# Kernel optimization log

Measured on AMD Instinct MI355X. Metric: run time of the kernel, lower is better.

## Reference

```python
import jax, jax.numpy as jnp
import numpy as np

HIDDEN = 2048
NUM_HEADS = 16
HEAD_DIM = HIDDEN // NUM_HEADS
SCALE = 1.0 / np.sqrt(HEAD_DIM).astype(np.float32)
BATCH, SEQ = 2, 2048


def setup_inputs() -> dict:
    key = jax.random.key(0)
    ks = jax.random.split(key, 9)
    std = 0.02
    inp = {
        'hidden_states': jax.random.normal(ks[0], (BATCH, SEQ, HIDDEN), jnp.float32),
        'attention_mask': jnp.zeros((BATCH, 1, 1, SEQ), jnp.float32),
        'Wq': jax.random.normal(ks[1], (HIDDEN, HIDDEN), jnp.float32) * std,
        'bq': jnp.zeros((HIDDEN,), jnp.float32),
        'Wk': jax.random.normal(ks[2], (HIDDEN, HIDDEN), jnp.float32) * std,
        'bk': jnp.zeros((HIDDEN,), jnp.float32),
        'Wv': jax.random.normal(ks[3], (HIDDEN, HIDDEN), jnp.float32) * std,
        'bv': jnp.zeros((HIDDEN,), jnp.float32),
        'Wo': jax.random.normal(ks[4], (HIDDEN, HIDDEN), jnp.float32) * std,
        'bo': jnp.zeros((HIDDEN,), jnp.float32),
    }
    return inp


def _split_heads(x):
    b, s, _ = x.shape
    return x.reshape(b, s, NUM_HEADS, HEAD_DIM).transpose(0, 2, 1, 3)  # [b,h,s,d]


def reference(hidden_states, attention_mask, Wq, bq, Wk, bk, Wv, bv, Wo, bo):
    # Linear layers (torch convention: y = x @ W.T + b)
    q = _split_heads(hidden_states @ Wq.T + bq)
    k = _split_heads(hidden_states @ Wk.T + bk)
    v = _split_heads(hidden_states @ Wv.T + bv)
    scores = jnp.einsum('bhqd,bhkd->bhqk', q, k) * SCALE
    scores = scores + attention_mask
    weights = jax.nn.softmax(scores, axis=-1)  # dropout is identity in eval
    ctx = jnp.einsum('bhqk,bhkd->bhqd', weights, v)
    b, h, s, d = ctx.shape
    ctx = ctx.transpose(0, 2, 1, 3).reshape(b, s, HIDDEN)
    return ctx @ Wo.T + bo
```

## Files before the change

kernel.cpp:

```cpp
#include <hip/hip_runtime.h>
#include <math.h>

typedef __bf16 bf16_t;
typedef bf16_t bf16x8 __attribute__((ext_vector_type(8)));
typedef float f32x4 __attribute__((ext_vector_type(4)));

#define HIDDEN 2048
#define SEQ 2048
#define BATCH 2
#define NHEADS 16
#define HDIM 128
#define MTOT (BATCH*SEQ)
#define SCALE 0.088388347648318447f

typedef __attribute__((address_space(1))) const void gvoid_t;
typedef __attribute__((address_space(3))) void svoid_t;
__device__ __forceinline__ void async_copy16(const bf16_t* g, bf16_t* l) {
  __builtin_amdgcn_global_load_lds((gvoid_t*)g, (svoid_t*)l, 16, 0, 0);
}

__global__ void cvt_f32_bf16(const float* __restrict__ in, bf16_t* __restrict__ out, int n4) {
  int i = blockIdx.x * 256 + threadIdx.x;
  if (i >= n4) return;
  float4 v = reinterpret_cast<const float4*>(in)[i];
  union { bf16_t h[4]; uint2 u; } t;
  t.h[0] = (bf16_t)v.x; t.h[1] = (bf16_t)v.y; t.h[2] = (bf16_t)v.z; t.h[3] = (bf16_t)v.w;
  reinterpret_cast<uint2*>(out)[i] = t.u;
}

__global__ void pack_bias2(const float* __restrict__ a, const float* __restrict__ b2,
                           float* __restrict__ out) {
  int i = blockIdx.x * 256 + threadIdx.x;
  out[i] = (i < HIDDEN) ? a[i] : b2[i - HIDDEN];
}

template<bool OUT_BF16, bool ROW_BIAS>
__global__ __launch_bounds__(256, 2)
void gemm_bt(const bf16_t* __restrict__ A, const bf16_t* __restrict__ Bt,
             const float* __restrict__ bias, void* __restrict__ Yv,
             int M, int N, int K, int ldY) {
  __shared__ __align__(16) bf16_t As[128 * 32];
  __shared__ __align__(16) bf16_t Bs[128 * 32];
  const int tid  = threadIdx.x;
  const int lane = tid & 63;
  const int wv   = tid >> 6;
  const int wr   = wv >> 1, wc = wv & 1;
  const int lr   = lane & 15, quad = lane >> 4;
  const int n0   = blockIdx.x * 128;
  const int m0   = blockIdx.y * 128;

  f32x4 acc[4][4] = {};

  const int srow = wv * 16 + (lane >> 2);
  const int scol = (lane & 3) * 8;
  const bf16_t* gA = A  + (size_t)(m0 + srow) * K + scol;
  const bf16_t* gB = Bt + (size_t)(n0 + srow) * K + scol;
  bf16_t* lA = &As[wv * 16 * 32];
  bf16_t* lB = &Bs[wv * 16 * 32];
  const size_t step64 = (size_t)64 * K;

  for (int kt = 0; kt < K; kt += 32) {
    __syncthreads();
    async_copy16(gA,          lA);
    async_copy16(gA + step64, lA + 64 * 32);
    async_copy16(gB,          lB);
    async_copy16(gB + step64, lB + 64 * 32);
    gA += 32; gB += 32;
    __syncthreads();
    bf16x8 af[4], bfr[4];
#pragma unroll
    for (int mi = 0; mi < 4; ++mi)
      af[mi] = *(const bf16x8*)&As[(wr * 64 + mi * 16 + lr) * 32 + quad * 8];
#pragma unroll
    for (int ni = 0; ni < 4; ++ni)
      bfr[ni] = *(const bf16x8*)&Bs[(wc * 64 + ni * 16 + lr) * 32 + quad * 8];
#pragma unroll
    for (int mi = 0; mi < 4; ++mi)
#pragma unroll
      for (int ni = 0; ni < 4; ++ni)
        acc[mi][ni] = __builtin_amdgcn_mfma_f32_16x16x32_bf16(af[mi], bfr[ni], acc[mi][ni], 0, 0, 0);
  }

  float bcol[4];
  if (!ROW_BIAS) {
#pragma unroll
    for (int ni = 0; ni < 4; ++ni) bcol[ni] = bias[n0 + wc * 64 + ni * 16 + lr];
  }
#pragma unroll
  for (int mi = 0; mi < 4; ++mi) {
#pragma unroll
    for (int r = 0; r < 4; ++r) {
      int row = m0 + wr * 64 + mi * 16 + quad * 4 + r;
      float brow = ROW_BIAS ? bias[row] : 0.0f;
      size_t base = (size_t)row * ldY + n0 + wc * 64;
#pragma unroll
      for (int ni = 0; ni < 4; ++ni) {
        float y = acc[mi][ni][r] + (ROW_BIAS ? brow : bcol[ni]);
        int col = ni * 16 + lr;
        if (OUT_BF16) ((bf16_t*)Yv)[base + col] = (bf16_t)y;
        else          ((float*)Yv)[base + col]  = y;
      }
    }
  }
}

#define BQ 64
#define BKV 64
#define LDQK 4096

__global__ __launch_bounds__(256, 4)
void attn_kernel(const bf16_t* __restrict__ QK, const bf16_t* __restrict__ Vt,
                 const float* __restrict__ mask, bf16_t* __restrict__ O) {
  __shared__ __align__(16) bf16_t Ks[BKV * 128];
  __shared__ __align__(16) bf16_t Vs[HDIM * BKV];
  __shared__ __align__(16) bf16_t Ps[BQ * BKV];

  const int tid  = threadIdx.x;
  const int lane = tid & 63;
  const int wv   = tid >> 6;
  const int lr   = lane & 15, quad = lane >> 4;
  const int q0   = blockIdx.x * BQ;
  const int bh   = blockIdx.y;
  const int b    = bh >> 4, h = bh & 15;

  const bf16_t* Qg = QK + (size_t)(b * SEQ + q0) * LDQK + h * HDIM;
  const bf16_t* Kg = QK + (size_t)(b * SEQ) * LDQK + HIDDEN + h * HDIM;
  const bf16_t* Vg = Vt + (size_t)(h * HDIM) * MTOT + b * SEQ;
  const float*  mb = mask + b * SEQ;

  bf16x8 qf[4];
#pragma unroll
  for (int dk = 0; dk < 4; ++dk)
    qf[dk] = *(const bf16x8*)(Qg + (size_t)(wv * 16 + lr) * LDQK + dk * 32 + quad * 8);

  const int krl = lane >> 4, kcs = lane & 15;
  const bf16_t* kg[4];
  bf16_t* lK[4];
#pragma unroll
  for (int i = 0; i < 4; ++i) {
    int row = wv * 16 + i * 4 + krl;
    kg[i] = Kg + (size_t)row * LDQK + ((kcs ^ (row & 15)) * 8);
    lK[i] = &Ks[(wv * 16 + i * 4) * 128];
  }
  const int vrl = lane >> 3, vcs = lane & 7;
  const bf16_t* vg[4];
  bf16_t* lV[4];
#pragma unroll
  for (int i = 0; i < 4; ++i) {
    int d = wv * 32 + i * 8 + vrl;
    vg[i] = Vg + (size_t)d * MTOT + ((vcs ^ (d & 7)) * 8);
    lV[i] = &Vs[(wv * 32 + i * 8) * BKV];
  }

  float l_st[4] = {0.0f, 0.0f, 0.0f, 0.0f};
  f32x4 oacc[8] = {};

  for (int kt = 0; kt < SEQ; kt += BKV) {
    __syncthreads();
#pragma unroll
    for (int i = 0; i < 4; ++i) async_copy16(kg[i] + (size_t)kt * LDQK, lK[i]);
#pragma unroll
    for (int i = 0; i < 4; ++i) async_copy16(vg[i] + kt, lV[i]);
    __syncthreads();

    float mk[4];
#pragma unroll
    for (int ni = 0; ni < 4; ++ni) mk[ni] = mb[kt + ni * 16 + lr];

    f32x4 sacc[4] = {};
#pragma unroll
    for (int dk = 0; dk < 4; ++dk) {
      bf16x8 kf[4];
#pragma unroll
      for (int ni = 0; ni < 4; ++ni)
        kf[ni] = *(const bf16x8*)&Ks[(ni * 16 + lr) * 128 + (((dk * 4 + quad) ^ lr) * 8)];
#pragma unroll
      for (int ni = 0; ni < 4; ++ni)
        sacc[ni] = __builtin_amdgcn_mfma_f32_16x16x32_bf16(qf[dk], kf[ni], sacc[ni], 0, 0, 0);
    }

#pragma unroll
    for (int r = 0; r < 4; ++r) {
      float p0 = __expf(fmaf(sacc[0][r], SCALE, mk[0]));
      float p1 = __expf(fmaf(sacc[1][r], SCALE, mk[1]));
      float p2 = __expf(fmaf(sacc[2][r], SCALE, mk[2]));
      float p3 = __expf(fmaf(sacc[3][r], SCALE, mk[3]));
      int pr = wv * 16 + quad * 4 + r;
      int key = pr & 7;
      Ps[pr * BKV + (((0 + (lr >> 3)) ^ key) * 8) + (lr & 7)] = (bf16_t)p0;
      Ps[pr * BKV + (((2 + (lr >> 3)) ^ key) * 8) + (lr & 7)] = (bf16_t)p1;
      Ps[pr * BKV + (((4 + (lr >> 3)) ^ key) * 8) + (lr & 7)] = (bf16_t)p2;
      Ps[pr * BKV + (((6 + (lr >> 3)) ^ key) * 8) + (lr & 7)] = (bf16_t)p3;
      l_st[r] += (p0 + p1) + (p2 + p3);
    }

#pragma unroll
    for (int ki = 0; ki < 2; ++ki) {
      bf16x8 pf = *(const bf16x8*)&Ps[(wv * 16 + lr) * BKV + (((ki * 4 + quad) ^ (lr & 7)) * 8)];
#pragma unroll
      for (int di = 0; di < 8; ++di) {
        bf16x8 vf = *(const bf16x8*)&Vs[(di * 16 + lr) * BKV + (((ki * 4 + quad) ^ (lr & 7)) * 8)];
        oacc[di] = __builtin_amdgcn_mfma_f32_16x16x32_bf16(pf, vf, oacc[di], 0, 0, 0);
      }
    }
  }

  bf16_t* Ob = O + (size_t)(b * SEQ + q0) * HIDDEN + h * HDIM;
#pragma unroll
  for (int r = 0; r < 4; ++r) {
    float s = l_st[r];
    s += __shfl_xor(s, 1);
    s += __shfl_xor(s, 2);
    s += __shfl_xor(s, 4);
    s += __shfl_xor(s, 8);
    float inv = 1.0f / s;
    size_t rowoff = (size_t)(wv * 16 + quad * 4 + r) * HIDDEN;
#pragma unroll
    for (int di = 0; di < 8; ++di)
      Ob[rowoff + di * 16 + lr] = (bf16_t)(oacc[di][r] * inv);
  }
}

extern "C" void kernel_launch(void* const* d_in, const int* in_sizes, int n_in,
                              void* d_out, int out_size, void* d_ws, size_t ws_size,
                              hipStream_t stream) {
  const float* x   = (const float*)d_in[0];
  const float* msk = (const float*)d_in[1];
  const float* Wq  = (const float*)d_in[2];
  const float* bq  = (const float*)d_in[3];
  const float* Wk  = (const float*)d_in[4];
  const float* bk  = (const float*)d_in[5];
  const float* Wv  = (const float*)d_in[6];
  const float* bv  = (const float*)d_in[7];
  const float* Wo  = (const float*)d_in[8];
  const float* bo  = (const float*)d_in[9];
  float* out = (float*)d_out;

  bf16_t* Xb   = (bf16_t*)d_ws;
  bf16_t* Wqkb = Xb   + (size_t)MTOT * HIDDEN;
  bf16_t* Wvb  = Wqkb + (size_t)2 * HIDDEN * HIDDEN;
  bf16_t* Wob  = Wvb  + (size_t)HIDDEN * HIDDEN;
  bf16_t* QKo  = Wob  + (size_t)HIDDEN * HIDDEN;
  bf16_t* Vto  = QKo  + (size_t)MTOT * 2 * HIDDEN;
  float*  bqk  = (float*)(Vto + (size_t)HIDDEN * MTOT);
  bf16_t* Cb   = Xb;

  const int n4x = MTOT * HIDDEN / 4;
  const int n4w = HIDDEN * HIDDEN / 4;
  cvt_f32_bf16<<<n4x / 256, 256, 0, stream>>>(x,  Xb, n4x);
  cvt_f32_bf16<<<n4w / 256, 256, 0, stream>>>(Wq, Wqkb, n4w);
  cvt_f32_bf16<<<n4w / 256, 256, 0, stream>>>(Wk, Wqkb + (size_t)HIDDEN * HIDDEN, n4w);
  cvt_f32_bf16<<<n4w / 256, 256, 0, stream>>>(Wv, Wvb, n4w);
  cvt_f32_bf16<<<n4w / 256, 256, 0, stream>>>(Wo, Wob, n4w);
  pack_bias2<<<2 * HIDDEN / 256, 256, 0, stream>>>(bq, bk, bqk);

  gemm_bt<true, false><<<dim3(32, 32), 256, 0, stream>>>(Xb, Wqkb, bqk, QKo,
                                                         MTOT, 2 * HIDDEN, HIDDEN, 2 * HIDDEN);
  gemm_bt<true, true><<<dim3(32, 16), 256, 0, stream>>>(Wvb, Xb, bv, Vto,
                                                        HIDDEN, MTOT, HIDDEN, MTOT);
  attn_kernel<<<dim3(SEQ / BQ, BATCH * NHEADS), 256, 0, stream>>>(QKo, Vto, msk, Cb);
  gemm_bt<false, false><<<dim3(16, 32), 256, 0, stream>>>(Cb, Wob, bo, out,
                                                          MTOT, HIDDEN, HIDDEN, HIDDEN);
}
```

Baseline: 428.4 us.

## Register-prefetch K/V tiles in attention, use exp2, merge conversion kernels

The attention kernel now loads the next K/V tile into registers while the current tile is being computed, then writes it to LDS after the barrier. This replaces the synchronous global-to-LDS async copies, with the aim of hiding global-memory latency behind the MFMA work. The exponent now uses a hardware exp2 with log2e folded into the scale and mask. The five f32-to-bf16 conversion launches are merged into a single 2D-grid kernel to cut launch overhead. The prefetch raises register pressure and adds an explicit LDS store step.

Result: slower. 753.3 us (+75.8%).

```diff
diff --git a/kernel.cpp b/kernel.cpp
--- a/kernel.cpp
+++ b/kernel.cpp
@@ -1,5 +1,4 @@
 #include <hip/hip_runtime.h>
-#include <math.h>
 
 typedef __bf16 bf16_t;
 typedef bf16_t bf16x8 __attribute__((ext_vector_type(8)));
@@ -12,6 +11,10 @@
 #define HDIM 128
 #define MTOT (BATCH*SEQ)
 #define SCALE 0.088388347648318447f
+#define C1EXP2 0.12753102158508967f
+#define LOG2E  1.4426950408889634f
+
+__device__ __forceinline__ float dev_exp2(float x) { return __builtin_amdgcn_exp2f(x); }
 
 typedef __attribute__((address_space(1))) const void gvoid_t;
 typedef __attribute__((address_space(3))) void svoid_t;
@@ -19,13 +22,26 @@
   __builtin_amdgcn_global_load_lds((gvoid_t*)g, (svoid_t*)l, 16, 0, 0);
 }
 
-__global__ void cvt_f32_bf16(const float* __restrict__ in, bf16_t* __restrict__ out, int n4) {
+__global__ void cvt_all(const float* __restrict__ x,  const float* __restrict__ wq,
+                        const float* __restrict__ wk, const float* __restrict__ wv,
+                        const float* __restrict__ wo,
+                        bf16_t* __restrict__ xb, bf16_t* __restrict__ wqkb,
+                        bf16_t* __restrict__ wvb, bf16_t* __restrict__ wob) {
+  const size_t HH = (size_t)HIDDEN * HIDDEN;
+  const float* src; bf16_t* dst;
+  switch (blockIdx.y) {
+    case 0:  src = x;        dst = xb;        break;
+    case 1:  src = x + HH;   dst = xb + HH;   break;
+    case 2:  src = wq;       dst = wqkb;      break;
+    case 3:  src = wk;       dst = wqkb + HH; break;
+    case 4:  src = wv;       dst = wvb;       break;
+    default: src = wo;       dst = wob;       break;
+  }
   int i = blockIdx.x * 256 + threadIdx.x;
-  if (i >= n4) return;
-  float4 v = reinterpret_cast<const float4*>(in)[i];
+  float4 v = reinterpret_cast<const float4*>(src)[i];
   union { bf16_t h[4]; uint2 u; } t;
   t.h[0] = (bf16_t)v.x; t.h[1] = (bf16_t)v.y; t.h[2] = (bf16_t)v.z; t.h[3] = (bf16_t)v.w;
-  reinterpret_cast<uint2*>(out)[i] = t.u;
+  reinterpret_cast<uint2*>(dst)[i] = t.u;
 }
 
 __global__ void pack_bias2(const float* __restrict__ a, const float* __restrict__ b2,
@@ -134,22 +150,25 @@
     qf[dk] = *(const bf16x8*)(Qg + (size_t)(wv * 16 + lr) * LDQK + dk * 32 + quad * 8);
 
   const int krl = lane >> 4, kcs = lane & 15;
-  const bf16_t* kg[4];
-  bf16_t* lK[4];
+  const int vrl = lane >> 3, vcs = lane & 7;
+  int lKa[4], lVa[4];
+  const bf16_t* kgp[4];
+  const bf16_t* vgp[4];
 #pragma unroll
   for (int i = 0; i < 4; ++i) {
     int row = wv * 16 + i * 4 + krl;
-    kg[i] = Kg + (size_t)row * LDQK + ((kcs ^ (row & 15)) * 8);
-    lK[i] = &Ks[(wv * 16 + i * 4) * 128];
-  }
-  const int vrl = lane >> 3, vcs = lane & 7;
-  const bf16_t* vg[4];
-  bf16_t* lV[4];
+    lKa[i] = row * 128 + ((kcs ^ (row & 15)) * 8);
+    kgp[i] = Kg + (size_t)row * LDQK + kcs * 8;
+    int d = wv * 32 + i * 8 + vrl;
+    lVa[i] = d * BKV + ((vcs ^ (d & 7)) * 8);
+    vgp[i] = Vg + (size_t)d * MTOT + vcs * 8;
+  }
+
+  uint4 kreg[4], vreg[4];
 #pragma unroll
   for (int i = 0; i < 4; ++i) {
-    int d = wv * 32 + i * 8 + vrl;
-    vg[i] = Vg + (size_t)d * MTOT + ((vcs ^ (d & 7)) * 8);
-    lV[i] = &Vs[(wv * 32 + i * 8) * BKV];
+    kreg[i] = *(const uint4*)(kgp[i]);
+    vreg[i] = *(const uint4*)(vgp[i]);
   }
 
   float l_st[4] = {0.0f, 0.0f, 0.0f, 0.0f};
@@ -158,14 +177,22 @@
   for (int kt = 0; kt < SEQ; kt += BKV) {
     __syncthreads();
 #pragma unroll
-    for (int i = 0; i < 4; ++i) async_copy16(kg[i] + (size_t)kt * LDQK, lK[i]);
-#pragma unroll
-    for (int i = 0; i < 4; ++i) async_copy16(vg[i] + kt, lV[i]);
-    __syncthreads();
+    for (int i = 0; i < 4; ++i) *(uint4*)&Ks[lKa[i]] = kreg[i];
+#pragma unroll
+    for (int i = 0; i < 4; ++i) *(uint4*)&Vs[lVa[i]] = vreg[i];
+    __syncthreads();
+
+    if (kt + BKV < SEQ) {
+#pragma unroll
+      for (int i = 0; i < 4; ++i) {
+        kreg[i] = *(const uint4*)(kgp[i] + (size_t)(kt + BKV) * LDQK);
+        vreg[i] = *(const uint4*)(vgp[i] + (kt + BKV));
+      }
+    }
 
     float mk[4];
 #pragma unroll
-    for (int ni = 0; ni < 4; ++ni) mk[ni] = mb[kt + ni * 16 + lr];
+    for (int ni = 0; ni < 4; ++ni) mk[ni] = mb[kt + ni * 16 + lr] * LOG2E;
 
     f32x4 sacc[4] = {};
 #pragma unroll
@@ -181,10 +208,10 @@
 
 #pragma unroll
     for (int r = 0; r < 4; ++r) {
-      float p0 = __expf(fmaf(sacc[0][r], SCALE, mk[0]));
-      float p1 = __expf(fmaf(sacc[1][r], SCALE, mk[1]));
-      float p2 = __expf(fmaf(sacc[2][r], SCALE, mk[2]));
-      float p3 = __expf(fmaf(sacc[3][r], SCALE, mk[3]));
+      float p0 = dev_exp2(fmaf(sacc[0][r], C1EXP2, mk[0]));
+      float p1 = dev_exp2(fmaf(sacc[1][r], C1EXP2, mk[1]));
+      float p2 = dev_exp2(fmaf(sacc[2][r], C1EXP2, mk[2]));
+      float p3 = dev_exp2(fmaf(sacc[3][r], C1EXP2, mk[3]));
       int pr = wv * 16 + quad * 4 + r;
       int key = pr & 7;
       Ps[pr * BKV + (((0 + (lr >> 3)) ^ key) * 8) + (lr & 7)] = (bf16_t)p0;
@@ -245,13 +272,8 @@
   float*  bqk  = (float*)(Vto + (size_t)HIDDEN * MTOT);
   bf16_t* Cb   = Xb;
 
-  const int n4x = MTOT * HIDDEN / 4;
-  const int n4w = HIDDEN * HIDDEN / 4;
-  cvt_f32_bf16<<<n4x / 256, 256, 0, stream>>>(x,  Xb, n4x);
-  cvt_f32_bf16<<<n4w / 256, 256, 0, stream>>>(Wq, Wqkb, n4w);
-  cvt_f32_bf16<<<n4w / 256, 256, 0, stream>>>(Wk, Wqkb + (size_t)HIDDEN * HIDDEN, n4w);
-  cvt_f32_bf16<<<n4w / 256, 256, 0, stream>>>(Wv, Wvb, n4w);
-  cvt_f32_bf16<<<n4w / 256, 256, 0, stream>>>(Wo, Wob, n4w);
+  cvt_all<<<dim3(HIDDEN * HIDDEN / 4 / 256, 6), 256, 0, stream>>>(
+      x, Wq, Wk, Wv, Wo, Xb, Wqkb, Wvb, Wob);
   pack_bias2<<<2 * HIDDEN / 256, 256, 0, stream>>>(bq, bk, bqk);
 
   gemm_bt<true, false><<<dim3(32, 32), 256, 0, stream>>>(Xb, Wqkb, bqk, QKo,
```
